# Optimization experiments

Measured on AMD Instinct MI355X. Metric: run time of the kernel, lower is better.

## Reference

```python
import jax, jax.numpy as jnp
import numpy as np

STATE_DIM = 512
HIDDEN = 256
ACTION = 8
BATCH = 32768
LN_EPS = 1e-5


def setup_inputs() -> dict:
    key = jax.random.key(0)
    ks = jax.random.split(key, 24)
    s = 0.02
    inp = {
        'initial_state': jax.random.normal(ks[0], (BATCH, STATE_DIM), jnp.float32),
        'final_state': jax.random.normal(ks[1], (BATCH, STATE_DIM), jnp.float32),
        'horizon': 10,
        # fc: Linear(1024->256), LayerNorm(256), ReLU, Linear(256->256), ReLU
        'W1': jax.random.normal(ks[2], (HIDDEN, 2 * STATE_DIM), jnp.float32) * s,
        'b1': jnp.zeros((HIDDEN,), jnp.float32),
        'ln_g': jnp.ones((HIDDEN,), jnp.float32),
        'ln_b': jnp.zeros((HIDDEN,), jnp.float32),
        'W2': jax.random.normal(ks[3], (HIDDEN, HIDDEN), jnp.float32) * s,
        'b2': jnp.zeros((HIDDEN,), jnp.float32),
        # GRU layer 0 (input=ACTION) and layer 1 (input=HIDDEN)
        'Wih0': jax.random.normal(ks[4], (3 * HIDDEN, ACTION), jnp.float32) * s,
        'Whh0': jax.random.normal(ks[5], (3 * HIDDEN, HIDDEN), jnp.float32) * s,
        'bih0': jnp.zeros((3 * HIDDEN,), jnp.float32),
        'bhh0': jnp.zeros((3 * HIDDEN,), jnp.float32),
        'Wih1': jax.random.normal(ks[6], (3 * HIDDEN, HIDDEN), jnp.float32) * s,
        'Whh1': jax.random.normal(ks[7], (3 * HIDDEN, HIDDEN), jnp.float32) * s,
        'bih1': jnp.zeros((3 * HIDDEN,), jnp.float32),
        'bhh1': jnp.zeros((3 * HIDDEN,), jnp.float32),
        # fc_action: 256 -> 8
        'Wa': jax.random.normal(ks[8], (ACTION, HIDDEN), jnp.float32) * s,
        'ba': jnp.zeros((ACTION,), jnp.float32),
        # fc_init_hidden: 256 -> 512
        'Winit': jax.random.normal(ks[9], (2 * HIDDEN, HIDDEN), jnp.float32) * s,
        'binit': jnp.zeros((2 * HIDDEN,), jnp.float32),
    }
    return inp


def _gru_cell(x, h, Wih, Whh, bih, bhh):
    # torch.nn.GRU cell: gates ordered [r, z, n]
    gi = x @ Wih.T + bih              # [B, 3H]
    gh = h @ Whh.T + bhh              # [B, 3H]
    i_r, i_z, i_n = jnp.split(gi, 3, axis=-1)
    h_r, h_z, h_n = jnp.split(gh, 3, axis=-1)
    r = jax.nn.sigmoid(i_r + h_r)
    z = jax.nn.sigmoid(i_z + h_z)
    n = jnp.tanh(i_n + r * h_n)
    return (1.0 - z) * n + z * h


def reference(initial_state, final_state, horizon, W1, b1, ln_g, ln_b, W2, b2,
              Wih0, Whh0, bih0, bhh0, Wih1, Whh1, bih1, bhh1, Wa, ba, Winit, binit):
    B = initial_state.shape[0]
    combined = jnp.concatenate([initial_state, final_state], axis=-1)  # [B, 2*state]
    h = combined @ W1.T + b1
    mu = jnp.mean(h, axis=-1, keepdims=True)
    var = jnp.var(h, axis=-1, keepdims=True)
    h = (h - mu) * jax.lax.rsqrt(var + LN_EPS) * ln_g + ln_b
    h = jax.nn.relu(h)
    h = jax.nn.relu(h @ W2.T + b2)    # [B, H]

    # Replicates torch .view(2, B, H) on a [B, 2H] tensor (row-major reshape)
    hidden = jnp.reshape(h @ Winit.T + binit, (2, B, HIDDEN))
    h0, h1 = hidden[0], hidden[1]
    a0 = jnp.zeros((B, ACTION), initial_state.dtype)

    def step(carry, _):
        h0, h1, a = carry
        h0n = _gru_cell(a, h0, Wih0, Whh0, bih0, bhh0)
        h1n = _gru_cell(h0n, h1, Wih1, Whh1, bih1, bhh1)
        logits = h1n @ Wa.T + ba       # [B, A]
        a_next = jax.nn.softmax(logits, axis=-1)
        return (h0n, h1n, a_next), logits

    _, logits_seq = jax.lax.scan(step, (h0, h1, a0), None, length=horizon)
    return jnp.transpose(logits_seq, (1, 0, 2))  # [B, horizon, A]
```

## Files before the change

### kernel.cpp

```cpp
#include <hip/hip_runtime.h>


#define HS 264

typedef __attribute__((ext_vector_type(8))) short short8;
typedef __attribute__((ext_vector_type(4))) float fvec4;

__device__ __forceinline__ float bf2f(unsigned short u) {
    union { unsigned int u; float f; } x; x.u = ((unsigned int)u) << 16; return x.f;
}
__device__ __forceinline__ unsigned short f2bf(float f) {
    union { float f; unsigned int u; } x; x.f = f;
    unsigned int r = x.u + 0x7fffu + ((x.u >> 16) & 1u);
    return (unsigned short)(r >> 16);
}
__device__ __forceinline__ float sigm(float x)   { return __builtin_amdgcn_rcpf(1.f + __expf(-x)); }
__device__ __forceinline__ float tanh_f(float x) { return 2.f * __builtin_amdgcn_rcpf(1.f + __expf(-2.f * x)) - 1.f; }

__device__ __forceinline__ short8 ld8(const unsigned short* p) {
    return *reinterpret_cast<const short8*>(p);
}
__device__ __forceinline__ fvec4 mfma16(short8 a, short8 b, fvec4 c) {
    return __builtin_amdgcn_mfma_f32_16x16x32_bf16(a, b, c, 0, 0, 0);
}
__device__ __forceinline__ fvec4 splat4(float v) {
    fvec4 r = {v, v, v, v}; return r;
}

__device__ __forceinline__ int packoff(int e, int K) {
    const int n = e / K, k = e % K;
    return (((n >> 4) * (K >> 5) + (k >> 5)) << 9)
         + (((((k >> 3) & 3) << 4) | (n & 15)) << 3) + (k & 7);
}

__global__ __launch_bounds__(256) void k_prep(
    const float* __restrict__ W1, const float* __restrict__ W2,
    const float* __restrict__ Winit, const float* __restrict__ Wih0,
    const float* __restrict__ Whh0, const float* __restrict__ Wih1,
    const float* __restrict__ Whh1, const float* __restrict__ Wa,
    unsigned short* __restrict__ wb)
{
    int i = blockIdx.x * 256 + threadIdx.x;
    if (i >= 1056768) return;
    float v; int dst;
    if (i < 262144) {
        v = W1[i];                dst = packoff(i, 1024);
    } else if (i < 327680) {
        int e = i - 262144;  v = W2[e];    dst = 262144 + packoff(e, 256);
    } else if (i < 458752) {
        int e = i - 327680;  v = Winit[e]; dst = 327680 + packoff(e, 256);
    } else if (i < 464896) {
        v = Wih0[i - 458752];     dst = i;
    } else if (i < 661504) {
        int e = i - 464896;  v = Whh0[e];  dst = 464896 + packoff(e, 256);
    } else if (i < 858112) {
        int e = i - 661504;  v = Wih1[e];  dst = 661504 + packoff(e, 256);
    } else if (i < 1054720) {
        int e = i - 858112;  v = Whh1[e];  dst = 858112 + packoff(e, 256);
    } else {
        v = Wa[i - 1054720];      dst = i;
    }
    wb[dst] = f2bf(v);
}

__global__ __launch_bounds__(512, 2) void k_encode(
    const float* __restrict__ ini, const float* __restrict__ fin,
    const unsigned short* __restrict__ W1b, const float* __restrict__ b1,
    const float* __restrict__ lng, const float* __restrict__ lnb,
    const unsigned short* __restrict__ W2b, const float* __restrict__ b2,
    const unsigned short* __restrict__ Winitb, const float* __restrict__ binit,
    unsigned short* __restrict__ h0g, unsigned short* __restrict__ h1g)
{
    __shared__ unsigned short hb[64 * HS];
    __shared__ unsigned short at[2][64 * 40];
    __shared__ float ps[64][8][2];
    __shared__ float st[64][2];
    const int tid = threadIdx.x, lane = tid & 63, w = tid >> 6;
    const int l15 = lane & 15, q = lane >> 4;
    const int rows0 = blockIdx.x * 64;
    const int c0 = w * 32;
    const fvec4 fz = {0.f, 0.f, 0.f, 0.f};

    const int srow = tid >> 3, sseg = (tid & 7) * 4;

    fvec4 acc[4][2];
#pragma unroll
    for (int rt = 0; rt < 4; ++rt) { acc[rt][0] = fz; acc[rt][1] = fz; }
    {
        const float* src0 = ini + (rows0 + srow) * 512 + sseg;
        fvec4 v = *reinterpret_cast<const fvec4*>(src0);
        union { unsigned short s[4]; unsigned long long u; } p;
        p.s[0] = f2bf(v[0]); p.s[1] = f2bf(v[1]); p.s[2] = f2bf(v[2]); p.s[3] = f2bf(v[3]);
        *reinterpret_cast<unsigned long long*>(&at[0][srow * 40 + sseg]) = p.u;
    }
    __syncthreads();
#pragma unroll 1
    for (int kc = 0; kc < 32; ++kc) {
        const int buf = kc & 1;
        if (kc < 31) {
            const int k0 = (kc + 1) * 32 + sseg;
            const float* src = (k0 < 512) ? (ini + (rows0 + srow) * 512 + k0)
                                          : (fin + (rows0 + srow) * 512 + (k0 - 512));
            fvec4 v = *reinterpret_cast<const fvec4*>(src);
            union { unsigned short s[4]; unsigned long long u; } p;
            p.s[0] = f2bf(v[0]); p.s[1] = f2bf(v[1]); p.s[2] = f2bf(v[2]); p.s[3] = f2bf(v[3]);
            *reinterpret_cast<unsigned long long*>(&at[buf ^ 1][srow * 40 + sseg]) = p.u;
        }
        short8 b8a = ld8(W1b + (((w * 2 + 0) * 32 + kc) * 64 + lane) * 8);
        short8 b8b = ld8(W1b + (((w * 2 + 1) * 32 + kc) * 64 + lane) * 8);
        short8 a8[4];
#pragma unroll
        for (int rt = 0; rt < 4; ++rt)
            a8[rt] = ld8(&at[buf][(rt * 16 + l15) * 40 + q * 8]);
#pragma unroll
        for (int rt = 0; rt < 4; ++rt) {
            acc[rt][0] = mfma16(a8[rt], b8a, acc[rt][0]);
            acc[rt][1] = mfma16(a8[rt], b8b, acc[rt][1]);
        }
        __syncthreads();
    }
    float bv[2] = { b1[c0 + l15], b1[c0 + 16 + l15] };
#pragma unroll
    for (int rt = 0; rt < 4; ++rt)
#pragma unroll
        for (int r = 0; r < 4; ++r) {
            float s = 0.f, s2 = 0.f;
#pragma unroll
            for (int ct = 0; ct < 2; ++ct) {
                float v = acc[rt][ct][r] + bv[ct];
                acc[rt][ct][r] = v;
                s += v; s2 += v * v;
            }
#pragma unroll
            for (int off = 1; off < 16; off <<= 1) {
                s  += __shfl_xor(s,  off, 64);
                s2 += __shfl_xor(s2, off, 64);
            }
            if (l15 == 0) {
                int row = rt * 16 + q * 4 + r;
                ps[row][w][0] = s; ps[row][w][1] = s2;
            }
        }
    __syncthreads();
    if (tid < 64) {
        float s = 0.f, s2 = 0.f;
#pragma unroll
        for (int j = 0; j < 8; ++j) { s += ps[tid][j][0]; s2 += ps[tid][j][1]; }
        float mu = s * (1.f / 256.f);
        float var = s2 * (1.f / 256.f) - mu * mu;
        st[tid][0] = mu; st[tid][1] = rsqrtf(var + 1e-5f);
    }
    __syncthreads();
    {
        float gv[2]  = { lng[c0 + l15], lng[c0 + 16 + l15] };
        float bbv[2] = { lnb[c0 + l15], lnb[c0 + 16 + l15] };
#pragma unroll
        for (int rt = 0; rt < 4; ++rt)
#pragma unroll
            for (int ct = 0; ct < 2; ++ct)
#pragma unroll
                for (int r = 0; r < 4; ++r) {
                    int row = rt * 16 + q * 4 + r;
                    float v = (acc[rt][ct][r] - st[row][0]) * st[row][1] * gv[ct] + bbv[ct];
                    v = fmaxf(v, 0.f);
                    hb[row * HS + c0 + ct * 16 + l15] = f2bf(v);
                }
    }
    __syncthreads();
    fvec4 acc2[4][2];
#pragma unroll
    for (int rt = 0; rt < 4; ++rt) { acc2[rt][0] = fz; acc2[rt][1] = fz; }
#pragma unroll 2
    for (int kc = 0; kc < 8; ++kc) {
        const int k0 = kc * 32 + q * 8;
        short8 a8[4];
#pragma unroll
        for (int rt = 0; rt < 4; ++rt) a8[rt] = ld8(hb + (rt * 16 + l15) * HS + k0);
#pragma unroll
        for (int ct = 0; ct < 2; ++ct) {
            short8 b8 = ld8(W2b + (((w * 2 + ct) * 8 + kc) * 64 + lane) * 8);
#pragma unroll
            for (int rt = 0; rt < 4; ++rt) acc2[rt][ct] = mfma16(a8[rt], b8, acc2[rt][ct]);
        }
    }
    {
        float b2v[2] = { b2[c0 + l15], b2[c0 + 16 + l15] };
        unsigned short stg[4][2][4];
#pragma unroll
        for (int rt = 0; rt < 4; ++rt)
#pragma unroll
            for (int ct = 0; ct < 2; ++ct)
#pragma unroll
                for (int r = 0; r < 4; ++r)
                    stg[rt][ct][r] = f2bf(fmaxf(acc2[rt][ct][r] + b2v[ct], 0.f));
        __syncthreads();
#pragma unroll
        for (int rt = 0; rt < 4; ++rt)
#pragma unroll
            for (int ct = 0; ct < 2; ++ct)
#pragma unroll
                for (int r = 0; r < 4; ++r)
                    hb[(rt * 16 + q * 4 + r) * HS + c0 + ct * 16 + l15] = stg[rt][ct][r];
    }
    __syncthreads();
    fvec4 a3[4][4];
#pragma unroll
    for (int rt = 0; rt < 4; ++rt)
#pragma unroll
        for (int ct = 0; ct < 4; ++ct) a3[rt][ct] = fz;
#pragma unroll 1
    for (int kc = 0; kc < 8; ++kc) {
        const int k0 = kc * 32 + q * 8;
        short8 a8[4];
#pragma unroll
        for (int rt = 0; rt < 4; ++rt) a8[rt] = ld8(hb + (rt * 16 + l15) * HS + k0);
#pragma unroll
        for (int ct = 0; ct < 4; ++ct) {
            short8 b8 = ld8(Winitb + (((w * 4 + ct) * 8 + kc) * 64 + lane) * 8);
#pragma unroll
            for (int rt = 0; rt < 4; ++rt) a3[rt][ct] = mfma16(a8[rt], b8, a3[rt][ct]);
        }
    }
    const int c0i = w * 64;
#pragma unroll
    for (int ct = 0; ct < 4; ++ct) {
        const int j = c0i + ct * 16 + l15;
        const float bz = binit[j];
        const int half = j >> 8, cc = j & 255;
#pragma unroll
        for (int rt = 0; rt < 4; ++rt)
#pragma unroll
            for (int r = 0; r < 4; ++r) {
                const int i = rows0 + rt * 16 + q * 4 + r;
                const unsigned short v = f2bf(a3[rt][ct][r] + bz);
                if (i < 16384) h0g[(2 * i + half) * 256 + cc] = v;
                else           h1g[(2 * (i - 16384) + half) * 256 + cc] = v;
            }
    }
}

__global__ __launch_bounds__(1024, 4) void k_roll(
    const unsigned short* __restrict__ h0g, const unsigned short* __restrict__ h1g,
    const unsigned short* __restrict__ Wih0b, const unsigned short* __restrict__ Whh0b,
    const unsigned short* __restrict__ Wih1b, const unsigned short* __restrict__ Whh1b,
    const unsigned short* __restrict__ Wab,
    const float* __restrict__ bih0, const float* __restrict__ bhh0,
    const float* __restrict__ bih1, const float* __restrict__ bhh1,
    const float* __restrict__ ba, float* __restrict__ out)
{
    __shared__ unsigned short h0sb[2][64 * HS];
    __shared__ unsigned short h1sb[2][64 * HS];
    __shared__ unsigned short avs[64 * 8];
    __shared__ float ldsb[2048];
    const int tid = threadIdx.x, lane = tid & 63, w = tid >> 6;
    const int l15 = lane & 15, q = lane >> 4;
    const int rows0 = blockIdx.x * 64;
    const int c = w * 16 + l15;
    const fvec4 fz = {0.f, 0.f, 0.f, 0.f};
    const short8 z8 = {0,0,0,0,0,0,0,0};

    for (int it = tid; it < 64 * 32; it += 1024) {
        const int row = it >> 5, g = (it & 31) * 8;
        *reinterpret_cast<short8*>(&h0sb[0][row * HS + g]) = ld8(h0g + (rows0 + row) * 256 + g);
        *reinterpret_cast<short8*>(&h1sb[0][row * HS + g]) = ld8(h1g + (rows0 + row) * 256 + g);
    }
    if (tid < 256) {
        const int j = tid;
        ldsb[j]       = bih0[j] + bhh0[j];
        ldsb[256 + j] = bih0[256 + j] + bhh0[256 + j];
        ldsb[512 + j] = bih0[512 + j];
        ldsb[768 + j] = bhh0[512 + j];
    } else if (tid < 512) {
        const int j = tid - 256;
        ldsb[1024 + j] = bih1[j] + bhh1[j];
        ldsb[1280 + j] = bih1[256 + j] + bhh1[256 + j];
        ldsb[1536 + j] = bih1[512 + j];
        ldsb[1792 + j] = bhh1[512 + j];
    }
    const float bav = ba[l15 & 7];
    __syncthreads();

    for (int t = 0; t < 10; ++t) {
        const int cur = t & 1, nxt = cur ^ 1;
        const unsigned short* h0c = h0sb[cur];
        unsigned short*       h0n = h0sb[nxt];
        const unsigned short* h1c = h1sb[cur];
        unsigned short*       h1n = h1sb[nxt];
        if (t > 0 && w < 4) {
            fvec4 f = fz;
#pragma unroll 1
            for (int kc = 0; kc < 8; ++kc) {
                const int k0 = kc * 32 + q * 8;
                short8 a8 = ld8(h1c + (w * 16 + l15) * HS + k0);
                short8 b8 = ld8(Wab + (l15 & 7) * 256 + k0);
                f = mfma16(a8, b8, f);
            }
#pragma unroll
            for (int r = 0; r < 4; ++r) {
                float s = f[r] + bav;
                float m = s;
                m = fmaxf(m, __shfl_xor(m, 1, 64));
                m = fmaxf(m, __shfl_xor(m, 2, 64));
                m = fmaxf(m, __shfl_xor(m, 4, 64));
                float e = __expf(s - m);
                float se = e;
                se += __shfl_xor(se, 1, 64);
                se += __shfl_xor(se, 2, 64);
                se += __shfl_xor(se, 4, 64);
                if (l15 < 8) {
                    const int lrow = w * 16 + q * 4 + r;
                    out[(rows0 + lrow) * 80 + (t - 1) * 8 + l15] = s;
                    avs[lrow * 8 + l15] = f2bf(e * __builtin_amdgcn_rcpf(se));
                }
            }
        }
        fvec4 aR[4], aZ[4], aNi[4], aNh[4];
        {
            const float vr = ldsb[c],       vz = ldsb[256 + c];
            const float vi = ldsb[512 + c], vh = ldsb[768 + c];
#pragma unroll
            for (int rt = 0; rt < 4; ++rt) {
                aR[rt]  = splat4(vr);
                aZ[rt]  = splat4(vz);
                aNi[rt] = splat4(vi);
                aNh[rt] = splat4(vh);
            }
        }
#pragma unroll 2
        for (int kc = 0; kc < 8; ++kc) {
            const int k0 = kc * 32 + q * 8;
            const unsigned short* wp =
                Whh0b + (((w * 8 + kc) * 64 + lane) * 8);
            const short8 wr = ld8(wp);
            const short8 wz = ld8(wp + 65536);
            const short8 wn = ld8(wp + 131072);
#pragma unroll
            for (int rt = 0; rt < 4; ++rt) {
                const short8 ah = ld8(h0c + (rt * 16 + l15) * HS + k0);
                aR[rt]  = mfma16(ah, wr, aR[rt]);
                aZ[rt]  = mfma16(ah, wz, aZ[rt]);
                aNh[rt] = mfma16(ah, wn, aNh[rt]);
            }
        }
        __syncthreads();
        if (t > 0) {
            const unsigned short* wp = Wih0b + c * 8;
            const short8 wr = ld8(wp);
            const short8 wz = ld8(wp + 2048);
            const short8 wn = ld8(wp + 4096);
#pragma unroll
            for (int rt = 0; rt < 4; ++rt) {
                short8 v = ld8(avs + (rt * 16 + l15) * 8);
                const short8 av = (q == 0) ? v : z8;
                aR[rt]  = mfma16(av, wr, aR[rt]);
                aZ[rt]  = mfma16(av, wz, aZ[rt]);
                aNi[rt] = mfma16(av, wn, aNi[rt]);
            }
        }
#pragma unroll
        for (int rt = 0; rt < 4; ++rt)
#pragma unroll
            for (int r = 0; r < 4; ++r) {
                const int row = rt * 16 + q * 4 + r;
                const float hold = bf2f(h0c[row * HS + c]);
                const float rr = sigm(aR[rt][r]);
                const float zz = sigm(aZ[rt][r]);
                const float nn = tanh_f(aNi[rt][r] + rr * aNh[rt][r]);
                h0n[row * HS + c] = f2bf((1.f - zz) * nn + zz * hold);
            }
        __syncthreads();
        {
            fvec4 bR[4], bZ[4], bNi[4], bNh[4];
            {
                const float vr = ldsb[1024 + c], vz = ldsb[1280 + c];
                const float vi = ldsb[1536 + c], vh = ldsb[1792 + c];
#pragma unroll
                for (int rt = 0; rt < 4; ++rt) {
                    bR[rt]  = splat4(vr);
                    bZ[rt]  = splat4(vz);
                    bNi[rt] = splat4(vi);
                    bNh[rt] = splat4(vh);
                }
            }
#pragma unroll 2
            for (int kc = 0; kc < 8; ++kc) {
                const int k0 = kc * 32 + q * 8;
                const unsigned short* wi =
                    Wih1b + (((w * 8 + kc) * 64 + lane) * 8);
                const short8 wir = ld8(wi);
                const short8 wiz = ld8(wi + 65536);
                const short8 win = ld8(wi + 131072);
#pragma unroll
                for (int rt = 0; rt < 4; ++rt) {
                    const short8 ai = ld8(h0n + (rt * 16 + l15) * HS + k0);
                    bR[rt]  = mfma16(ai, wir, bR[rt]);
                    bZ[rt]  = mfma16(ai, wiz, bZ[rt]);
                    bNi[rt] = mfma16(ai, win, bNi[rt]);
                }
            }
#pragma unroll 2
            for (int kc = 0; kc < 8; ++kc) {
                const int k0 = kc * 32 + q * 8;
                const unsigned short* wh =
                    Whh1b + (((w * 8 + kc) * 64 + lane) * 8);
                const short8 whr = ld8(wh);
                const short8 whz = ld8(wh + 65536);
                const short8 whn = ld8(wh + 131072);
#pragma unroll
                for (int rt = 0; rt < 4; ++rt) {
                    const short8 ah = ld8(h1c + (rt * 16 + l15) * HS + k0);
                    bR[rt]  = mfma16(ah, whr, bR[rt]);
                    bZ[rt]  = mfma16(ah, whz, bZ[rt]);
                    bNh[rt] = mfma16(ah, whn, bNh[rt]);
                }
            }
#pragma unroll
            for (int rt = 0; rt < 4; ++rt)
#pragma unroll
                for (int r = 0; r < 4; ++r) {
                    const int row = rt * 16 + q * 4 + r;
                    const float hold = bf2f(h1c[row * HS + c]);
                    const float rr = sigm(bR[rt][r]);
                    const float zz = sigm(bZ[rt][r]);
                    const float nn = tanh_f(bNi[rt][r] + rr * bNh[rt][r]);
                    h1n[row * HS + c] = f2bf((1.f - zz) * nn + zz * hold);
                }
        }
        __syncthreads();
    }
    if (w < 4) {
        const unsigned short* h1f = h1sb[0];
        fvec4 f = fz;
#pragma unroll 1
        for (int kc = 0; kc < 8; ++kc) {
            const int k0 = kc * 32 + q * 8;
            short8 a8 = ld8(h1f + (w * 16 + l15) * HS + k0);
            short8 b8 = ld8(Wab + (l15 & 7) * 256 + k0);
            f = mfma16(a8, b8, f);
        }
#pragma unroll
        for (int r = 0; r < 4; ++r) {
            if (l15 < 8) {
                const int lrow = w * 16 + q * 4 + r;
                out[(rows0 + lrow) * 80 + 72 + l15] = f[r] + bav;
            }
        }
    }
}

extern "C" void kernel_launch(void* const* d_in, const int* in_sizes, int n_in,
                              void* d_out, int out_size, void* d_ws, size_t ws_size,
                              hipStream_t stream)
{
    const float* ini   = (const float*)d_in[0];
    const float* fin   = (const float*)d_in[1];
    const float* W1    = (const float*)d_in[3];
    const float* b1    = (const float*)d_in[4];
    const float* lng   = (const float*)d_in[5];
    const float* lnb   = (const float*)d_in[6];
    const float* W2    = (const float*)d_in[7];
    const float* b2    = (const float*)d_in[8];
    const float* Wih0  = (const float*)d_in[9];
    const float* Whh0  = (const float*)d_in[10];
    const float* bih0  = (const float*)d_in[11];
    const float* bhh0  = (const float*)d_in[12];
    const float* Wih1  = (const float*)d_in[13];
    const float* Whh1  = (const float*)d_in[14];
    const float* bih1  = (const float*)d_in[15];
    const float* bhh1  = (const float*)d_in[16];
    const float* Wa    = (const float*)d_in[17];
    const float* ba    = (const float*)d_in[18];
    const float* Winit = (const float*)d_in[19];
    const float* binit = (const float*)d_in[20];
    float* out = (float*)d_out;

    char* ws = (char*)d_ws;
    unsigned short* wb     = (unsigned short*)ws;
    unsigned short* W1b    = wb;
    unsigned short* W2b    = wb + 262144;
    unsigned short* Winitb = wb + 327680;
    unsigned short* Wih0b  = wb + 458752;
    unsigned short* Whh0b  = wb + 464896;
    unsigned short* Wih1b  = wb + 661504;
    unsigned short* Whh1b  = wb + 858112;
    unsigned short* Wab    = wb + 1054720;
    unsigned short* h0g = (unsigned short*)(ws + 2113536);
    unsigned short* h1g = (unsigned short*)(ws + 18890752);

    k_prep<<<dim3(4128), dim3(256), 0, stream>>>(W1, W2, Winit, Wih0, Whh0, Wih1, Whh1, Wa, wb);
    k_encode<<<dim3(512), dim3(512), 0, stream>>>(ini, fin, W1b, b1, lng, lnb, W2b, b2,
                                                  Winitb, binit, h0g, h1g);
    k_roll<<<dim3(512), dim3(1024), 0, stream>>>(h0g, h1g, Wih0b, Whh0b, Wih1b, Whh1b, Wab,
                                                 bih0, bhh0, bih1, bhh1, ba, out);
}
```

Before: 681.2 us.

## Stream GRU weights into LDS asynchronously with double buffering and single h buffers

Replaces the direct global loads of the r/z weight fragments with asynchronous global_load_lds transfers into a per-wave double-buffered LDS staging area. The next k-chunk is prefetched while the current one runs through MFMA, and the n-gate fragment is software-pipelined in registers, with explicit vmcnt waits. The h0/h1 ping-pong buffers become single in-place buffers. Layer 1 is reordered to do its recurrent (Whh1) product before the barrier and its input (Wih1) product after it. The aim is to hide global/L2 latency on weight fetches within the same LDS budget, at the cost of hand-written waitcnt ordering that is fragile.

```diff
diff --git a/kernel.cpp b/kernel.cpp
--- a/kernel.cpp
+++ b/kernel.cpp
@@ -25,6 +25,11 @@
 }
 __device__ __forceinline__ fvec4 splat4(float v) {
     fvec4 r = {v, v, v, v}; return r;
+}
+__device__ __forceinline__ void gload16(const unsigned short* g, unsigned short* l) {
+    __builtin_amdgcn_global_load_lds(
+        (const __attribute__((address_space(1))) unsigned int*)g,
+        (__attribute__((address_space(3))) unsigned int*)l, 16, 0, 0);
 }
 
 __device__ __forceinline__ int packoff(int e, int K) {
@@ -248,10 +253,11 @@
     const float* __restrict__ bih1, const float* __restrict__ bhh1,
     const float* __restrict__ ba, float* __restrict__ out)
 {
-    __shared__ unsigned short h0sb[2][64 * HS];
-    __shared__ unsigned short h1sb[2][64 * HS];
+    __shared__ unsigned short h0s[64 * HS];
+    __shared__ unsigned short h1s[64 * HS];
     __shared__ unsigned short avs[64 * 8];
     __shared__ float ldsb[2048];
+    __shared__ unsigned short wst[32768];
     const int tid = threadIdx.x, lane = tid & 63, w = tid >> 6;
     const int l15 = lane & 15, q = lane >> 4;
     const int rows0 = blockIdx.x * 64;
@@ -259,10 +265,12 @@
     const fvec4 fz = {0.f, 0.f, 0.f, 0.f};
     const short8 z8 = {0,0,0,0,0,0,0,0};
 
+#define WSLOT(b, g) (wst + (((b) * 16 + w) * 2 + (g)) * 512)
+
     for (int it = tid; it < 64 * 32; it += 1024) {
         const int row = it >> 5, g = (it & 31) * 8;
-        *reinterpret_cast<short8*>(&h0sb[0][row * HS + g]) = ld8(h0g + (rows0 + row) * 256 + g);
-        *reinterpret_cast<short8*>(&h1sb[0][row * HS + g]) = ld8(h1g + (rows0 + row) * 256 + g);
+        *reinterpret_cast<short8*>(&h0s[row * HS + g]) = ld8(h0g + (rows0 + row) * 256 + g);
+        *reinterpret_cast<short8*>(&h1s[row * HS + g]) = ld8(h1g + (rows0 + row) * 256 + g);
     }
     if (tid < 256) {
         const int j = tid;
@@ -280,18 +288,19 @@
     const float bav = ba[l15 & 7];
     __syncthreads();
 
+    {
+        const unsigned short* g0 = Whh0b + ((w * 8 + 0) * 64 + lane) * 8;
+        gload16(g0,         WSLOT(0, 0));
+        gload16(g0 + 65536, WSLOT(0, 1));
+    }
+
     for (int t = 0; t < 10; ++t) {
-        const int cur = t & 1, nxt = cur ^ 1;
-        const unsigned short* h0c = h0sb[cur];
-        unsigned short*       h0n = h0sb[nxt];
-        const unsigned short* h1c = h1sb[cur];
-        unsigned short*       h1n = h1sb[nxt];
         if (t > 0 && w < 4) {
             fvec4 f = fz;
 #pragma unroll 1
             for (int kc = 0; kc < 8; ++kc) {
                 const int k0 = kc * 32 + q * 8;
-                short8 a8 = ld8(h1c + (w * 16 + l15) * HS + k0);
+                short8 a8 = ld8(h1s + (w * 16 + l15) * HS + k0);
                 short8 b8 = ld8(Wab + (l15 & 7) * 256 + k0);
                 f = mfma16(a8, b8, f);
             }
@@ -326,23 +335,48 @@
                 aNh[rt] = splat4(vh);
             }
         }
-#pragma unroll 2
-        for (int kc = 0; kc < 8; ++kc) {
-            const int k0 = kc * 32 + q * 8;
-            const unsigned short* wp =
-                Whh0b + (((w * 8 + kc) * 64 + lane) * 8);
-            const short8 wr = ld8(wp);
-            const short8 wz = ld8(wp + 65536);
-            const short8 wn = ld8(wp + 131072);
-#pragma unroll
-            for (int rt = 0; rt < 4; ++rt) {
-                const short8 ah = ld8(h0c + (rt * 16 + l15) * HS + k0);
-                aR[rt]  = mfma16(ah, wr, aR[rt]);
-                aZ[rt]  = mfma16(ah, wz, aZ[rt]);
-                aNh[rt] = mfma16(ah, wn, aNh[rt]);
+        {
+            short8 wn_nx = ld8(Whh0b + ((w * 8 + 0) * 64 + lane) * 8 + 131072);
+#pragma unroll 1
+            for (int kc = 0; kc < 7; ++kc) {
+                const short8 wn = wn_nx;
+                const unsigned short* g1 = Whh0b + ((w * 8 + kc + 1) * 64 + lane) * 8;
+                gload16(g1,         WSLOT((kc + 1) & 1, 0));
+                gload16(g1 + 65536, WSLOT((kc + 1) & 1, 1));
+                wn_nx = ld8(g1 + 131072);
+                asm volatile("s_waitcnt vmcnt(3)" ::: "memory");
+                const short8 wr = ld8(WSLOT(kc & 1, 0) + lane * 8);
+                const short8 wz = ld8(WSLOT(kc & 1, 1) + lane * 8);
+                const int k0 = kc * 32 + q * 8;
+#pragma unroll
+                for (int rt = 0; rt < 4; ++rt) {
+                    const short8 ah = ld8(h0s + (rt * 16 + l15) * HS + k0);
+                    aR[rt]  = mfma16(ah, wr, aR[rt]);
+                    aZ[rt]  = mfma16(ah, wz, aZ[rt]);
+                    aNh[rt] = mfma16(ah, wn, aNh[rt]);
+                }
+            }
+            {
+                const short8 wn = wn_nx;
+                asm volatile("s_waitcnt vmcnt(0)" ::: "memory");
+                const short8 wr = ld8(WSLOT(1, 0) + lane * 8);
+                const short8 wz = ld8(WSLOT(1, 1) + lane * 8);
+                const int k0 = 7 * 32 + q * 8;
+#pragma unroll
+                for (int rt = 0; rt < 4; ++rt) {
+                    const short8 ah = ld8(h0s + (rt * 16 + l15) * HS + k0);
+                    aR[rt]  = mfma16(ah, wr, aR[rt]);
+                    aZ[rt]  = mfma16(ah, wz, aZ[rt]);
+                    aNh[rt] = mfma16(ah, wn, aNh[rt]);
+                }
             }
         }
         __syncthreads();
+        {
+            const unsigned short* g0 = Whh1b + ((w * 8 + 0) * 64 + lane) * 8;
+            gload16(g0,         WSLOT(0, 0));
+            gload16(g0 + 65536, WSLOT(0, 1));
+        }
         if (t > 0) {
             const unsigned short* wp = Wih0b + c * 8;
             const short8 wr = ld8(wp);
@@ -362,79 +396,126 @@
 #pragma unroll
             for (int r = 0; r < 4; ++r) {
                 const int row = rt * 16 + q * 4 + r;
-                const float hold = bf2f(h0c[row * HS + c]);
+                const float hold = bf2f(h0s[row * HS + c]);
                 const float rr = sigm(aR[rt][r]);
                 const float zz = sigm(aZ[rt][r]);
                 const float nn = tanh_f(aNi[rt][r] + rr * aNh[rt][r]);
-                h0n[row * HS + c] = f2bf((1.f - zz) * nn + zz * hold);
-            }
+                h0s[row * HS + c] = f2bf((1.f - zz) * nn + zz * hold);
+            }
+        fvec4 bR[4], bZ[4], bNi[4], bNh[4];
+        {
+            const float vr = ldsb[1024 + c], vz = ldsb[1280 + c];
+            const float vi = ldsb[1536 + c], vh = ldsb[1792 + c];
+#pragma unroll
+            for (int rt = 0; rt < 4; ++rt) {
+                bR[rt]  = splat4(vr);
+                bZ[rt]  = splat4(vz);
+                bNi[rt] = splat4(vi);
+                bNh[rt] = splat4(vh);
+            }
+        }
+        {
+            short8 wn_nx = ld8(Whh1b + ((w * 8 + 0) * 64 + lane) * 8 + 131072);
+#pragma unroll 1
+            for (int kc = 0; kc < 7; ++kc) {
+                const short8 wn = wn_nx;
+                const unsigned short* g1 = Whh1b + ((w * 8 + kc + 1) * 64 + lane) * 8;
+                gload16(g1,         WSLOT((kc + 1) & 1, 0));
+                gload16(g1 + 65536, WSLOT((kc + 1) & 1, 1));
+                wn_nx = ld8(g1 + 131072);
+                asm volatile("s_waitcnt vmcnt(3)" ::: "memory");
+                const short8 wr = ld8(WSLOT(kc & 1, 0) + lane * 8);
+                const short8 wz = ld8(WSLOT(kc & 1, 1) + lane * 8);
+                const int k0 = kc * 32 + q * 8;
+#pragma unroll
+                for (int rt = 0; rt < 4; ++rt) {
+                    const short8 ah = ld8(h1s + (rt * 16 + l15) * HS + k0);
+                    bR[rt]  = mfma16(ah, wr, bR[rt]);
+                    bZ[rt]  = mfma16(ah, wz, bZ[rt]);
+                    bNh[rt] = mfma16(ah, wn, bNh[rt]);
+                }
+            }
+            {
+                const short8 wn = wn_nx;
+                asm volatile("s_waitcnt vmcnt(0)" ::: "memory");
+                const short8 wr = ld8(WSLOT(1, 0) + lane * 8);
+                const short8 wz = ld8(WSLOT(1, 1) + lane * 8);
+                const int k0 = 7 * 32 + q * 8;
+#pragma unroll
+                for (int rt = 0; rt < 4; ++rt) {
+                    const short8 ah = ld8(h1s + (rt * 16 + l15) * HS + k0);
+                    bR[rt]  = mfma16(ah, wr, bR[rt]);
+                    bZ[rt]  = mfma16(ah, wz, bZ[rt]);
+                    bNh[rt] = mfma16(ah, wn, bNh[rt]);
+                }
+            }
+        }
         __syncthreads();
         {
-            fvec4 bR[4], bZ[4], bNi[4], bNh[4];
+            const unsigned short* g0 = Wih1b + ((w * 8 + 0) * 64 + lane) * 8;
+            gload16(g0,         WSLOT(0, 0));
+            gload16(g0 + 65536, WSLOT(0, 1));
+        }
+        {
+            short8 wn_nx = ld8(Wih1b + ((w * 8 + 0) * 64 + lane) * 8 + 131072);
+#pragma unroll 1
+            for (int kc = 0; kc < 7; ++kc) {
+                const short8 wn = wn_nx;
+                const unsigned short* g1 = Wih1b + ((w * 8 + kc + 1) * 64 + lane) * 8;
+                gload16(g1,         WSLOT((kc + 1) & 1, 0));
+                gload16(g1 + 65536, WSLOT((kc + 1) & 1, 1));
+                wn_nx = ld8(g1 + 131072);
+                asm volatile("s_waitcnt vmcnt(3)" ::: "memory");
+                const short8 wr = ld8(WSLOT(kc & 1, 0) + lane * 8);
+                const short8 wz = ld8(WSLOT(kc & 1, 1) + lane * 8);
+                const int k0 = kc * 32 + q * 8;
+#pragma unroll
+                for (int rt = 0; rt < 4; ++rt) {
+                    const short8 ai = ld8(h0s + (rt * 16 + l15) * HS + k0);
+                    bR[rt]  = mfma16(ai, wr, bR[rt]);
+                    bZ[rt]  = mfma16(ai, wz, bZ[rt]);
+                    bNi[rt] = mfma16(ai, wn, bNi[rt]);
+                }
+            }
             {
-                const float vr = ldsb[1024 + c], vz = ldsb[1280 + c];
-                const float vi = ldsb[1536 + c], vh = ldsb[1792 + c];
+                const short8 wn = wn_nx;
+                asm volatile("s_waitcnt vmcnt(0)" ::: "memory");
+                const short8 wr = ld8(WSLOT(1, 0) + lane * 8);
+                const short8 wz = ld8(WSLOT(1, 1) + lane * 8);
+                const int k0 = 7 * 32 + q * 8;
 #pragma unroll
                 for (int rt = 0; rt < 4; ++rt) {
-                    bR[rt]  = splat4(vr);
-                    bZ[rt]  = splat4(vz);
-                    bNi[rt] = splat4(vi);
-                    bNh[rt] = splat4(vh);
-                }
-            }
-#pragma unroll 2
-            for (int kc = 0; kc < 8; ++kc) {
-                const int k0 = kc * 32 + q * 8;
-                const unsigned short* wi =
-                    Wih1b + (((w * 8 + kc) * 64 + lane) * 8);
-                const short8 wir = ld8(wi);
-                const short8 wiz = ld8(wi + 65536);
-                const short8 win = ld8(wi + 131072);
-#pragma unroll
-                for (int rt = 0; rt < 4; ++rt) {
-                    const short8 ai = ld8(h0n + (rt * 16 + l15) * HS + k0);
-                    bR[rt]  = mfma16(ai, wir, bR[rt]);
-                    bZ[rt]  = mfma16(ai, wiz, bZ[rt]);
-                    bNi[rt] = mfma16(ai, win, bNi[rt]);
-                }
-            }
-#pragma unroll 2
-            for (int kc = 0; kc < 8; ++kc) {
-                const int k0 = kc * 32 + q * 8;
-                const unsigned short* wh =
-                    Whh1b + (((w * 8 + kc) * 64 + lane) * 8);
-                const short8 whr = ld8(wh);
-                const short8 whz = ld8(wh + 65536);
-                const short8 whn = ld8(wh + 131072);
-#pragma unroll
-                for (int rt = 0; rt < 4; ++rt) {
-                    const short8 ah = ld8(h1c + (rt * 16 + l15) * HS + k0);
-                    bR[rt]  = mfma16(ah, whr, bR[rt]);
-                    bZ[rt]  = mfma16(ah, whz, bZ[rt]);
-                    bNh[rt] = mfma16(ah, whn, bNh[rt]);
-                }
-            }
-#pragma unroll
-            for (int rt = 0; rt < 4; ++rt)
-#pragma unroll
-                for (int r = 0; r < 4; ++r) {
-                    const int row = rt * 16 + q * 4 + r;
-                    const float hold = bf2f(h1c[row * HS + c]);
-                    const float rr = sigm(bR[rt][r]);
-                    const float zz = sigm(bZ[rt][r]);
-                    const float nn = tanh_f(bNi[rt][r] + rr * bNh[rt][r]);
-                    h1n[row * HS + c] = f2bf((1.f - zz) * nn + zz * hold);
-                }
-        }
+                    const short8 ai = ld8(h0s + (rt * 16 + l15) * HS + k0);
+                    bR[rt]  = mfma16(ai, wr, bR[rt]);
+                    bZ[rt]  = mfma16(ai, wz, bZ[rt]);
+                    bNi[rt] = mfma16(ai, wn, bNi[rt]);
+                }
+            }
+        }
+        {
+            const unsigned short* g0 = Whh0b + ((w * 8 + 0) * 64 + lane) * 8;
+            gload16(g0,         WSLOT(0, 0));
+            gload16(g0 + 65536, WSLOT(0, 1));
+        }
+#pragma unroll
+        for (int rt = 0; rt < 4; ++rt)
+#pragma unroll
+            for (int r = 0; r < 4; ++r) {
+                const int row = rt * 16 + q * 4 + r;
+                const float hold = bf2f(h1s[row * HS + c]);
+                const float rr = sigm(bR[rt][r]);
+                const float zz = sigm(bZ[rt][r]);
+                const float nn = tanh_f(bNi[rt][r] + rr * bNh[rt][r]);
+                h1s[row * HS + c] = f2bf((1.f - zz) * nn + zz * hold);
+            }
         __syncthreads();
     }
     if (w < 4) {
-        const unsigned short* h1f = h1sb[0];
         fvec4 f = fz;
 #pragma unroll 1
         for (int kc = 0; kc < 8; ++kc) {
             const int k0 = kc * 32 + q * 8;
-            short8 a8 = ld8(h1f + (w * 16 + l15) * HS + k0);
+            short8 a8 = ld8(h1s + (w * 16 + l15) * HS + k0);
             short8 b8 = ld8(Wab + (l15 & 7) * 256 + k0);
             f = mfma16(a8, b8, f);
         }
@@ -446,6 +527,7 @@
             }
         }
     }
+#undef WSLOT
 }
 
 extern "C" void kernel_launch(void* const* d_in, const int* in_sizes, int n_in,
```

After: 822.2 us. 1.21x slower.
